# Kernel optimization log

Measured on AMD Instinct MI355X. Metric: run time of the kernel, lower is better.

## Reference

```python
import jax, jax.numpy as jnp
import numpy as np

N, E, K, NELEM, NB, NG = 10000, 160000, 64, 10, 8, 16
R_MAX = 5.0
P_CUT = 5
AVG_NEI = 16.0
SQRT4PI = 3.5449077018110318


def real_sph_l3(u):
    # real spherical harmonics up to l=3 (orthonormal), u: unit vectors [E,3]
    x, y, z = u[..., 0], u[..., 1], u[..., 2]
    x2, y2, z2 = x * x, y * y, z * z
    Y = [
        0.28209479177387814 * jnp.ones_like(x),
        0.4886025119029199 * y, 0.4886025119029199 * z, 0.4886025119029199 * x,
        1.0925484305920792 * x * y, 1.0925484305920792 * y * z,
        0.31539156525252005 * (3.0 * z2 - 1.0),
        1.0925484305920792 * x * z, 0.5462742152960396 * (x2 - y2),
        0.5900435899266435 * y * (3.0 * x2 - y2), 2.890611442640554 * x * y * z,
        0.4570457994644658 * y * (5.0 * z2 - 1.0), 0.3731763325901154 * z * (5.0 * z2 - 3.0),
        0.4570457994644658 * x * (5.0 * z2 - 1.0), 1.445305721320277 * z * (x2 - y2),
        0.5900435899266435 * x * (x2 - 3.0 * y2),
    ]
    return jnp.stack(Y, axis=-1)  # [E,16]


def radial_embed(r):
    # Bessel radial basis * polynomial cutoff (p=5)
    n = jnp.arange(1, NB + 1, dtype=r.dtype)
    pref = jnp.sqrt(2.0 / R_MAX)
    bessel = pref * jnp.sin(n[None, :] * jnp.pi * r[:, None] / R_MAX) / r[:, None]
    u = r / R_MAX
    fcut = 1.0 - 21.0 * u**5 + 35.0 * u**6 - 15.0 * u**7
    fcut = jnp.where(u < 1.0, fcut, 0.0)
    return bessel * fcut[:, None]  # [E,NB]


L_SLICES = [(0, 1), (1, 4), (4, 9), (9, 16)]


def product_basis(A, Wp):
    # many-body invariant (ACE-style) features per channel from A: [N,K,16]
    A0 = A[:, :, 0]                                         # nu=1 invariant
    p = jnp.stack([jnp.sum(A[:, :, a:b] ** 2, axis=-1) for a, b in L_SLICES], axis=-1)  # nu=2 power spectrum [N,K,4]
    cub = A0 * p.sum(axis=-1)                               # nu=3 invariant
    inv = jnp.concatenate([A0[..., None], p, cub[..., None]], axis=-1)  # [N,K,6]
    return jnp.einsum('nkj,kj->nk', inv, Wp)


def energy_fn(positions, node_attrs, shifts, atomic_energies, embed_W, Wr1, Wr2, lin_up, Wp, W_read, edge_index, batch):
    sender, receiver = edge_index[0], edge_index[1]
    vec = positions[receiver] - positions[sender] + shifts   # [E,3]
    r = jnp.sqrt(jnp.sum(vec * vec, axis=-1) + 1e-12)        # [E]
    sh = real_sph_l3(vec / r[:, None]) * SQRT4PI             # [E,16]
    rb = radial_embed(r)                                     # [E,NB]
    e0 = jax.ops.segment_sum(node_attrs @ atomic_energies, batch, num_segments=NG)
    h = node_attrs @ embed_W                                 # [N,K]
    for i in range(2):
        hu = h @ lin_up[i]                                   # [N,K]
        R = jax.nn.silu(rb @ Wr1[i]) @ Wr2[i]                # [E,K*16]
        R = R.reshape(E, K, 16)
        msg = R * sh[:, None, :] * hu[sender][:, :, None]    # [E,K,16]
        A = jax.ops.segment_sum(msg, receiver, num_segments=N) / AVG_NEI  # [N,K,16]
        h = product_basis(A, Wp[i])                          # [N,K]
    node_e = h @ W_read                                      # [N]
    inter_e = jax.ops.segment_sum(node_e, batch, num_segments=NG)
    return e0 + inter_e                                      # [NG]


def setup_inputs() -> dict:
    key = jax.random.key(0)
    ks = jax.random.split(key, 12)
    positions = jax.random.normal(ks[0], (N, 3), dtype=jnp.float32) * 2.0
    species = jax.random.randint(ks[1], (N,), 0, NELEM)
    node_attrs = jax.nn.one_hot(species, NELEM, dtype=jnp.float32)
    edge_index = jax.random.randint(ks[2], (2, E), 0, N)
    shifts = jnp.zeros((E, 3), dtype=jnp.float32)
    batch = jnp.sort(jax.random.randint(ks[3], (N,), 0, NG))
    atomic_energies = -jnp.arange(1.0, NELEM + 1.0, dtype=jnp.float32)
    s = 0.1
    embed_W = jax.random.normal(ks[4], (NELEM, K), dtype=jnp.float32) * s
    Wr1 = jax.random.normal(ks[5], (2, NB, 64), dtype=jnp.float32) * s
    Wr2 = jax.random.normal(ks[6], (2, 64, K * 16), dtype=jnp.float32) * s
    lin_up = jax.random.normal(ks[7], (2, K, K), dtype=jnp.float32) * s
    Wp = jax.random.normal(ks[8], (2, K, 6), dtype=jnp.float32) * s
    W_read = jax.random.normal(ks[9], (K,), dtype=jnp.float32) * s
    return {
        'positions': positions, 'node_attrs': node_attrs, 'shifts': shifts,
        'edge_index': edge_index, 'batch': batch, 'num_graphs': NG,
        'atomic_energies': atomic_energies, 'embed_W': embed_W, 'Wr1': Wr1,
        'Wr2': Wr2, 'lin_up': lin_up, 'Wp': Wp, 'W_read': W_read,
    }


def reference(positions, node_attrs, shifts, edge_index, batch, num_graphs,
              atomic_energies, embed_W, Wr1, Wr2, lin_up, Wp, W_read):
    def e_of_pos(pos):
        return energy_fn(pos, node_attrs, shifts, atomic_energies, embed_W,
                         Wr1, Wr2, lin_up, Wp, W_read, edge_index, batch)
    energy = e_of_pos(positions)
    forces = -jax.grad(lambda p: e_of_pos(p).sum())(positions)
    return energy, forces
```

## Files before the change

kernel.cpp:

```cpp
#include <hip/hip_runtime.h>
#include <cmath>
#include <type_traits>
#include <utility>

#define NA 10000
#define NE 160000
#define KC 64
#define NEL 10
#define NBR 8
#define NGR 16
#define ECH 16

#define C0 0.28209479177387814f
#define C1 0.4886025119029199f
#define C2 1.0925484305920792f
#define C3 0.31539156525252005f
#define C4 0.5462742152960396f
#define C5 0.5900435899266435f
#define C6 2.890611442640554f
#define C7 0.4570457994644658f
#define C8 0.3731763325901154f
#define C9 1.445305721320277f
#define SQ4PI 3.5449077018110318f
#define PREF 0.6324555320336759f
#define PI_F 3.14159265358979323846f

typedef float f32x4 __attribute__((ext_vector_type(4)));
typedef short s16x8 __attribute__((ext_vector_type(8)));
typedef __bf16 b16x8 __attribute__((ext_vector_type(8)));

__device__ __forceinline__ float sigmoidf_(float x){ return 1.0f/(1.0f+expf(-x)); }

__device__ __forceinline__ unsigned short f2b(float f){
  unsigned int u = __float_as_uint(f);
  unsigned int r = u + 0x7FFFu + ((u>>16)&1u);
  return (unsigned short)(r>>16);
}

template<typename T, typename = void>
struct mfma_takes_short : std::false_type {};
template<typename T>
struct mfma_takes_short<T, std::void_t<decltype(__builtin_amdgcn_mfma_f32_16x16x32_bf16(
    std::declval<T>(), std::declval<T>(), std::declval<f32x4>(), 0, 0, 0))>> : std::true_type {};

__device__ __forceinline__ f32x4 mfma16(s16x8 a, s16x8 b, f32x4 c){
  if constexpr (mfma_takes_short<s16x8>::value)
    return __builtin_amdgcn_mfma_f32_16x16x32_bf16(a, b, c, 0, 0, 0);
  else
    return __builtin_amdgcn_mfma_f32_16x16x32_bf16(
        __builtin_bit_cast(b16x8, a), __builtin_bit_cast(b16x8, b), c, 0, 0, 0);
}

__global__ void edge_geom_k(const float* __restrict__ pos, const float* __restrict__ shifts,
                            const int* __restrict__ eidx,
                            float* __restrict__ vecb, float* __restrict__ rbuf,
                            float* __restrict__ shb, float* __restrict__ rbb){
  int e = blockIdx.x*blockDim.x + threadIdx.x;
  if (e >= NE) return;
  int sn = eidx[e], rc = eidx[NE+e];
  float vx = pos[rc*3+0]-pos[sn*3+0]+shifts[e*3+0];
  float vy = pos[rc*3+1]-pos[sn*3+1]+shifts[e*3+1];
  float vz = pos[rc*3+2]-pos[sn*3+2]+shifts[e*3+2];
  float r = sqrtf(vx*vx+vy*vy+vz*vz+1e-12f);
  vecb[e*3+0]=vx; vecb[e*3+1]=vy; vecb[e*3+2]=vz; rbuf[e]=r;
  float inv = 1.0f/r; float x=vx*inv,y=vy*inv,z=vz*inv;
  float x2=x*x,y2=y*y,z2=z*z;
  float Y[16];
  Y[0]=C0; Y[1]=C1*y; Y[2]=C1*z; Y[3]=C1*x;
  Y[4]=C2*x*y; Y[5]=C2*y*z; Y[6]=C3*(3.f*z2-1.f); Y[7]=C2*x*z; Y[8]=C4*(x2-y2);
  Y[9]=C5*y*(3.f*x2-y2); Y[10]=C6*x*y*z; Y[11]=C7*y*(5.f*z2-1.f);
  Y[12]=C8*z*(5.f*z2-3.f); Y[13]=C7*x*(5.f*z2-1.f); Y[14]=C9*z*(x2-y2);
  Y[15]=C5*x*(x2-3.f*y2);
  #pragma unroll
  for (int m=0;m<16;m++) shb[e*16+m] = Y[m]*SQ4PI;
  float u = r*0.2f;
  float fc = 0.f;
  if (u < 1.0f){ float u2=u*u,u4=u2*u2,u5=u4*u,u6=u5*u,u7=u6*u; fc = 1.f-21.f*u5+35.f*u6-15.f*u7; }
  #pragma unroll
  for (int b=0;b<NBR;b++){
    float a = (float)(b+1)*PI_F*0.2f;
    rbb[e*NBR+b] = PREF*sinf(a*r)*inv*fc;
  }
}

__global__ void embed_k(const float* __restrict__ attrs, const float* __restrict__ W, float* __restrict__ h0){
  int idx = blockIdx.x*blockDim.x+threadIdx.x;
  if (idx >= NA*KC) return;
  int n = idx>>6, k = idx&63;
  float s=0;
  #pragma unroll
  for (int j=0;j<NEL;j++) s += attrs[n*NEL+j]*W[j*KC+k];
  h0[idx]=s;
}

__global__ void hu_k(const float* __restrict__ h, const float* __restrict__ lin, float* __restrict__ out){
  int idx = blockIdx.x*blockDim.x+threadIdx.x;
  if (idx >= NA*KC) return;
  int n = idx>>6, k = idx&63;
  float s=0;
  for (int c=0;c<KC;c++) s += h[n*KC+c]*lin[c*KC+k];
  out[idx]=s;
}

__global__ void ghu_to_gh_k(const float* __restrict__ g, const float* __restrict__ lin, float* __restrict__ out){
  int idx = blockIdx.x*blockDim.x+threadIdx.x;
  if (idx >= NA*KC) return;
  int n = idx>>6, k = idx&63;
  float s=0;
  for (int c=0;c<KC;c++) s += g[n*KC+c]*lin[k*KC+c];
  out[idx]=s;
}

__global__ void count_k(const int* __restrict__ eidx, int* __restrict__ cnt){
  int e = blockIdx.x*blockDim.x+threadIdx.x;
  if (e<NE) atomicAdd(&cnt[eidx[NE+e]], 1);
}
__global__ void scan_k(const int* __restrict__ cnt, int* __restrict__ rs, int* __restrict__ fill){
  __shared__ int part[256];
  int t = threadIdx.x;
  const int PER = (NA + 255)/256;
  int base = t*PER;
  int s = 0;
  for (int j=0;j<PER;j++){ int i=base+j; if (i<NA) s += cnt[i]; }
  part[t] = s; __syncthreads();
  for (int off=1; off<256; off<<=1){
    int v = (t>=off) ? part[t-off] : 0;
    __syncthreads();
    part[t] += v;
    __syncthreads();
  }
  int run = (t==0) ? 0 : part[t-1];
  for (int j=0;j<PER;j++){ int i=base+j; if (i<NA){ rs[i]=run; fill[i]=run; run += cnt[i]; } }
  if (t==255) rs[NA]=run;
}
__global__ void place_k(const int* __restrict__ eidx, int* __restrict__ fill, int* __restrict__ perm){
  int e = blockIdx.x*blockDim.x+threadIdx.x;
  if (e>=NE) return;
  int r = eidx[NE+e];
  int p = atomicAdd(&fill[r],1);
  perm[p]=e;
}

__global__ void prep_w_k(const float* __restrict__ Wr2, unsigned short* __restrict__ w2b,
                         unsigned short* __restrict__ w2t){
  int idx = blockIdx.x*blockDim.x+threadIdx.x;
  if (idx >= 2*65536) return;
  int l = idx>>16;
  int rem = idx & 65535;
  int c = rem>>10, o = rem&1023;
  unsigned short v = f2b(Wr2[idx]);
  w2b[idx] = v;
  w2t[l*65536 + o*64 + c] = v;
}

__global__ __launch_bounds__(256) void fwd_A_k(const int* __restrict__ rs, const int* __restrict__ perm,
    const int* __restrict__ eidx, const float* __restrict__ shb, const float* __restrict__ rbb,
    const float* __restrict__ hu, const float* __restrict__ Wr1, const unsigned short* __restrict__ w2t,
    float* __restrict__ A){
  __shared__ __align__(16) unsigned short s_s[16*64];
  __shared__ float s_sh[16*17];
  __shared__ float s_hu[16*68];
  __shared__ float s_rb[16*8];
  __shared__ float s_w1[8*64];
  __shared__ int s_snd[16];
  int n = blockIdx.x, t = threadIdx.x;
  int lane = t & 63, w = t >> 6;
  int row = lane & 15, g = lane >> 4;
  int e0 = rs[n], e1 = rs[n+1];
  s_w1[t] = Wr1[t]; s_w1[256+t] = Wr1[256+t];
  float acc[16];
  #pragma unroll
  for (int i=0;i<16;i++) acc[i]=0.f;

  for (int ce=e0; ce<e1; ce+=ECH){
    int ne = min(ECH, e1-ce);
    __syncthreads();
    if (t<ECH) s_snd[t] = (t<ne) ? eidx[perm[ce+t]] : -1;
    { int le=t>>4, m=t&15; s_sh[le*17+m] = (le<ne) ? shb[perm[ce+le]*16+m] : 0.f; }
    if (t < ECH*NBR){ int le=t>>3, b=t&7; s_rb[le*8+b] = (le<ne) ? rbb[perm[ce+le]*NBR+b] : 0.f; }
    __syncthreads();
    #pragma unroll
    for (int q=0;q<4;q++){
      int idx=q*256+t; int le=idx>>6, c=idx&63;
      int sn = s_snd[le];
      s_hu[le*68+c] = (sn>=0) ? hu[sn*KC+c] : 0.f;
      float tt=0;
      #pragma unroll
      for (int b=0;b<NBR;b++) tt += s_rb[le*8+b]*s_w1[b*64+c];
      float sv = tt*sigmoidf_(tt);
      s_s[le*64 + (c ^ ((le&7)<<3))] = (sn>=0) ? f2b(sv) : (unsigned short)0;
    }
    __syncthreads();
    s16x8 a0 = *(const s16x8*)&s_s[row*64 + ((g*8)      ^ ((row&7)<<3))];
    s16x8 a1 = *(const s16x8*)&s_s[row*64 + ((32 + g*8) ^ ((row&7)<<3))];
    #pragma unroll 4
    for (int ot=0; ot<16; ot++){
      int otile = w*16 + ot;
      const unsigned short* bp = w2t + (otile*16 + row)*64 + g*8;
      s16x8 b0 = *(const s16x8*)(bp);
      s16x8 b1 = *(const s16x8*)(bp + 32);
      f32x4 d = {0.f,0.f,0.f,0.f};
      d = mfma16(a0, b0, d);
      d = mfma16(a1, b1, d);
      float s = 0.f;
      #pragma unroll
      for (int q=0;q<4;q++){
        int e = g*4+q;
        s += d[q] * s_sh[e*17+row] * s_hu[e*68+otile];
      }
      acc[ot] += s;
    }
  }
  const float inv16 = 1.f/16.f;
  #pragma unroll
  for (int ot=0; ot<16; ot++){
    float v = acc[ot];
    v += __shfl_xor(v, 16);
    v += __shfl_xor(v, 32);
    if (lane < 16) A[n*1024 + (w*16+ot)*16 + lane] = v*inv16;
  }
}

__global__ void pb_fwd_k(const float* __restrict__ A, const float* __restrict__ Wp, float* __restrict__ h){
  int idx = blockIdx.x*blockDim.x+threadIdx.x;
  if (idx>=NA*KC) return;
  int k = idx&63;
  const float* a = A + idx*16;
  float v[16];
  #pragma unroll
  for (int m=0;m<16;m++) v[m]=a[m];
  float p0 = v[0]*v[0];
  float p1 = v[1]*v[1]+v[2]*v[2]+v[3]*v[3];
  float p2 = v[4]*v[4]+v[5]*v[5]+v[6]*v[6]+v[7]*v[7]+v[8]*v[8];
  float p3 = 0.f;
  #pragma unroll
  for (int m=9;m<16;m++) p3 += v[m]*v[m];
  float P = p0+p1+p2+p3;
  const float* wp = Wp + k*6;
  h[idx] = v[0]*wp[0] + p0*wp[1] + p1*wp[2] + p2*wp[3] + p3*wp[4] + v[0]*P*wp[5];
}

__global__ void pb_bwd_k(const float* __restrict__ A, const float* __restrict__ Wp,
                         const float* __restrict__ gh, const float* __restrict__ Wread,
                         int useW, float* __restrict__ gA){
  int idx = blockIdx.x*blockDim.x+threadIdx.x;
  if (idx>=NA*KC) return;
  int k = idx&63;
  const float* a = A + idx*16;
  float v[16];
  #pragma unroll
  for (int m=0;m<16;m++) v[m]=a[m];
  float p0 = v[0]*v[0];
  float p1 = v[1]*v[1]+v[2]*v[2]+v[3]*v[3];
  float p2 = v[4]*v[4]+v[5]*v[5]+v[6]*v[6]+v[7]*v[7]+v[8]*v[8];
  float p3 = 0.f;
  #pragma unroll
  for (int m=9;m<16;m++) p3 += v[m]*v[m];
  float P = p0+p1+p2+p3;
  float g = useW ? Wread[k] : gh[idx];
  const float* wp = Wp + k*6;
  float w5a0 = wp[5]*v[0];
  float out[16];
  #pragma unroll
  for (int m=0;m<16;m++){
    int l = (m==0)?0:(m<4)?1:(m<9)?2:3;
    float r = 2.f*v[m]*(wp[1+l] + w5a0);
    if (m==0) r += wp[0] + wp[5]*P;
    out[m] = g*r;
  }
  float* d = gA + idx*16;
  #pragma unroll
  for (int m=0;m<16;m++) d[m]=out[m];
}

__global__ __launch_bounds__(256) void bwd_edge_k(const int* __restrict__ eidx,
    const float* __restrict__ shb, const float* __restrict__ rbb,
    const float* __restrict__ vecb, const float* __restrict__ rbuf,
    const float* __restrict__ hu, const float* __restrict__ Wr1,
    const unsigned short* __restrict__ w2b,
    const unsigned short* __restrict__ w2t,
    const float* __restrict__ gA, float* __restrict__ ghu, int do_ghu,
    float* __restrict__ gpos){
  __shared__ __align__(16) unsigned short s_s[16*64];
  __shared__ __align__(16) unsigned short s_gR[16*1024];
  __shared__ float s_sh[16*17];
  __shared__ float s_hu[16*68];
  __shared__ float s_rb[16*8];
  __shared__ float s_w1[8*64];
  __shared__ float s_gshp[4*16*17];
  __shared__ float s_gt[16*64];
  __shared__ float s_grb[16*8];
  __shared__ int s_snd[16], s_rcv[16];
  int t = threadIdx.x, lane = t&63, w = t>>6;
  int row = lane&15, g = lane>>4;
  int eb = blockIdx.x*ECH;
  const float inv16 = 1.f/16.f;

  s_w1[t] = Wr1[t]; s_w1[256+t] = Wr1[256+t];
  if (t<ECH){ s_snd[t]=eidx[eb+t]; s_rcv[t]=eidx[NE+eb+t]; }
  { int le=t>>4, m=t&15; s_sh[le*17+m]=shb[(eb+le)*16+m]; }
  if (t<ECH*NBR){ int le=t>>3, b=t&7; s_rb[le*8+b]=rbb[(eb+le)*NBR+b]; }
  __syncthreads();
  #pragma unroll
  for (int q=0;q<4;q++){
    int idx=q*256+t; int le=idx>>6, c=idx&63;
    s_hu[le*68+c]=hu[s_snd[le]*KC+c];
    float tt=0;
    #pragma unroll
    for (int b=0;b<NBR;b++) tt += s_rb[le*8+b]*s_w1[b*64+c];
    s_s[le*64 + (c ^ ((le&7)<<3))] = f2b(tt*sigmoidf_(tt));
  }
  __syncthreads();

  s16x8 a0 = *(const s16x8*)&s_s[row*64 + ((g*8)      ^ ((row&7)<<3))];
  s16x8 a1 = *(const s16x8*)&s_s[row*64 + ((32 + g*8) ^ ((row&7)<<3))];
  float gsh_acc[4] = {0.f,0.f,0.f,0.f};
  #pragma unroll 2
  for (int ot=0; ot<16; ot++){
    int k = w*16 + ot;
    const unsigned short* bp = w2t + (k*16 + row)*64 + g*8;
    s16x8 b0 = *(const s16x8*)(bp);
    s16x8 b1 = *(const s16x8*)(bp + 32);
    f32x4 d = {0.f,0.f,0.f,0.f};
    d = mfma16(a0, b0, d);
    d = mfma16(a1, b1, d);
    float gm[4], ghv[4];
    #pragma unroll
    for (int q=0;q<4;q++) gm[q] = gA[s_rcv[g*4+q]*1024 + k*16 + row]*inv16;
    #pragma unroll
    for (int q=0;q<4;q++){
      int e = g*4+q;
      float shv = s_sh[e*17+row];
      float huv = s_hu[e*68+k];
      float p = gm[q]*d[q];
      ghv[q] = p*shv;
      gsh_acc[q] += p*huv;
      float gr = gm[q]*shv*huv;
      s_gR[e*1024 + ((k*16+row) ^ ((e&7)<<3))] = f2b(gr);
    }
    if (do_ghu){
      #pragma unroll
      for (int off=1; off<16; off<<=1){
        ghv[0]+=__shfl_xor(ghv[0],off); ghv[1]+=__shfl_xor(ghv[1],off);
        ghv[2]+=__shfl_xor(ghv[2],off); ghv[3]+=__shfl_xor(ghv[3],off);
      }
      if (row==0){
        #pragma unroll
        for (int q=0;q<4;q++) atomicAdd(&ghu[s_snd[g*4+q]*KC + k], ghv[q]);
      }
    }
  }
  #pragma unroll
  for (int q=0;q<4;q++) s_gshp[w*272 + (g*4+q)*17 + row] = gsh_acc[q];
  __syncthreads();

  f32x4 dgs = {0.f,0.f,0.f,0.f};
  #pragma unroll 4
  for (int kb=0; kb<32; kb++){
    int kelem = kb*32 + g*8;
    s16x8 a = *(const s16x8*)&s_gR[row*1024 + (kelem ^ ((row&7)<<3))];
    s16x8 b = *(const s16x8*)&w2b[(w*16+row)*1024 + kelem];
    dgs = mfma16(a, b, dgs);
  }
  #pragma unroll
  for (int q=0;q<4;q++){
    int e = g*4+q, c = w*16+row;
    float tt=0;
    #pragma unroll
    for (int b=0;b<NBR;b++) tt += s_rb[e*8+b]*s_w1[b*64+c];
    float sg = sigmoidf_(tt);
    float ds = sg*(1.f+tt*(1.f-sg));
    s_gt[e*64 + c] = dgs[q]*ds;
  }
  __syncthreads();

  if (t < ECH*NBR){
    int le=t>>3, b=t&7;
    float s=0;
    for (int c=0;c<KC;c++) s += s_gt[le*64+c]*s_w1[b*64+c];
    s_grb[le*8+b]=s;
  }
  { int le=t>>4, m=t&15;
    s_gshp[le*17+m] = s_gshp[le*17+m]+s_gshp[272+le*17+m]+s_gshp[544+le*17+m]+s_gshp[816+le*17+m]; }
  __syncthreads();

  if (t < ECH){
    int le=t; int e=eb+le;
    float r = rbuf[e]; float inv=1.f/r;
    float vx=vecb[e*3+0], vy=vecb[e*3+1], vz=vecb[e*3+2];
    float x=vx*inv, y=vy*inv, z=vz*inv;
    float x2=x*x, y2=y*y, z2=z*z;
    float G[16];
    #pragma unroll
    for (int m=0;m<16;m++) G[m]=s_gshp[le*17+m];
    float gx = C1*G[3] + C2*(y*G[4]+z*G[7]) + 2.f*C4*x*G[8] + 6.f*C5*x*y*G[9]
             + C6*y*z*G[10] + C7*(5.f*z2-1.f)*G[13] + 2.f*C9*x*z*G[14] + 3.f*C5*(x2-y2)*G[15];
    float gy = C1*G[1] + C2*(x*G[4]+z*G[5]) - 2.f*C4*y*G[8] + 3.f*C5*(x2-y2)*G[9]
             + C6*x*z*G[10] + C7*(5.f*z2-1.f)*G[11] - 2.f*C9*y*z*G[14] - 6.f*C5*x*y*G[15];
    float gz = C1*G[2] + C2*(y*G[5]+x*G[7]) + 6.f*C3*z*G[6] + C6*x*y*G[10]
             + 10.f*C7*y*z*G[11] + C8*(15.f*z2-3.f)*G[12] + 10.f*C7*x*z*G[13] + C9*(x2-y2)*G[14];
    gx*=SQ4PI; gy*=SQ4PI; gz*=SQ4PI;
    float gr=0.f;
    float u=r*0.2f;
    if (u<1.f){
      float u2=u*u, u4=u2*u2, u5=u4*u, u6=u5*u, u7=u6*u;
      float fc=1.f-21.f*u5+35.f*u6-15.f*u7;
      float dfc=(-105.f*u4+210.f*u5-105.f*u6)*0.2f;
      #pragma unroll
      for (int b=0;b<NBR;b++){
        float a=(float)(b+1)*PI_F*0.2f;
        float sa=sinf(a*r), ca=cosf(a*r);
        float bes=PREF*sa*inv;
        float dbes=PREF*(a*ca*inv - sa*inv*inv);
        gr += s_grb[le*8+b]*(dbes*fc + bes*dfc);
      }
    }
    float dot = x*gx+y*gy+z*gz;
    float gvx = (gx - x*dot)*inv + gr*x;
    float gvy = (gy - y*dot)*inv + gr*y;
    float gvz = (gz - z*dot)*inv + gr*z;
    int sn=s_snd[le], rc=s_rcv[le];
    atomicAdd(&gpos[rc*3+0], gvx); atomicAdd(&gpos[rc*3+1], gvy); atomicAdd(&gpos[rc*3+2], gvz);
    atomicAdd(&gpos[sn*3+0], -gvx); atomicAdd(&gpos[sn*3+1], -gvy); atomicAdd(&gpos[sn*3+2], -gvz);
  }
}

__global__ void energy_k(const float* __restrict__ attrs, const float* __restrict__ ae,
                         const float* __restrict__ h2, const float* __restrict__ Wread,
                         const int* __restrict__ batch, float* __restrict__ out_e){
  int n = blockIdx.x*blockDim.x+threadIdx.x;
  if (n>=NA) return;
  float v=0;
  #pragma unroll
  for (int j=0;j<NEL;j++) v += attrs[n*NEL+j]*ae[j];
  float s=0;
  for (int kk=0;kk<KC;kk++) s += h2[n*KC+kk]*Wread[kk];
  atomicAdd(&out_e[batch[n]], v+s);
}
__global__ void forces_k(const float* __restrict__ gpos, float* __restrict__ out_f){
  int i = blockIdx.x*blockDim.x+threadIdx.x;
  if (i<NA*3) out_f[i] = -gpos[i];
}

extern "C" void kernel_launch(void* const* d_in, const int* in_sizes, int n_in,
                              void* d_out, int out_size, void* d_ws, size_t ws_size,
                              hipStream_t stream){
  const float* pos    = (const float*)d_in[0];
  const float* attrs  = (const float*)d_in[1];
  const float* shifts = (const float*)d_in[2];
  const int*   eidx   = (const int*)d_in[3];
  const int*   batch  = (const int*)d_in[4];
  const float* ae     = (const float*)d_in[6];
  const float* embedW = (const float*)d_in[7];
  const float* Wr1    = (const float*)d_in[8];
  const float* Wr2    = (const float*)d_in[9];
  const float* lin    = (const float*)d_in[10];
  const float* Wp     = (const float*)d_in[11];
  const float* Wread  = (const float*)d_in[12];
  float* out_e = (float*)d_out;
  float* out_f = out_e + NGR;

  char* w = (char*)d_ws;
  auto alloc = [&](size_t nElem)->void*{ void* p = (void*)w; w += ((nElem*4 + 255)/256)*256; return p; };
  float* vecb = (float*)alloc((size_t)3*NE);
  float* rbuf = (float*)alloc((size_t)NE);
  float* shb  = (float*)alloc((size_t)16*NE);
  float* rbb  = (float*)alloc((size_t)8*NE);
  float* h0   = (float*)alloc((size_t)NA*KC);
  float* h1   = (float*)alloc((size_t)NA*KC);
  float* h2   = (float*)alloc((size_t)NA*KC);
  float* hu1  = (float*)alloc((size_t)NA*KC);
  float* hu2  = (float*)alloc((size_t)NA*KC);
  float* gh1  = (float*)alloc((size_t)NA*KC);
  float* ghu2 = (float*)alloc((size_t)NA*KC);
  float* A1   = (float*)alloc((size_t)NA*1024);
  float* A2   = (float*)alloc((size_t)NA*1024);
  float* gA   = (float*)alloc((size_t)NA*1024);
  float* gpos = (float*)alloc((size_t)NA*3);
  unsigned short* w2b = (unsigned short*)alloc((size_t)2*65536);
  unsigned short* w2t = (unsigned short*)alloc((size_t)2*65536);
  int* cnt  = (int*)alloc((size_t)NA);
  int* rsar = (int*)alloc((size_t)NA+1);
  int* fill = (int*)alloc((size_t)NA);
  int* perm = (int*)alloc((size_t)NE);

  hipMemsetAsync(cnt, 0, NA*sizeof(int), stream);
  hipMemsetAsync(gpos, 0, NA*3*sizeof(float), stream);
  hipMemsetAsync(ghu2, 0, NA*KC*sizeof(float), stream);
  hipMemsetAsync(out_e, 0, NGR*sizeof(float), stream);

  prep_w_k<<<(2*65536+255)/256, 256, 0, stream>>>(Wr2, w2b, w2t);
  edge_geom_k<<<(NE+255)/256, 256, 0, stream>>>(pos, shifts, eidx, vecb, rbuf, shb, rbb);
  embed_k<<<(NA*KC+255)/256, 256, 0, stream>>>(attrs, embedW, h0);
  count_k<<<(NE+255)/256, 256, 0, stream>>>(eidx, cnt);
  scan_k<<<1, 256, 0, stream>>>(cnt, rsar, fill);
  place_k<<<(NE+255)/256, 256, 0, stream>>>(eidx, fill, perm);

  hu_k<<<(NA*KC+255)/256, 256, 0, stream>>>(h0, lin + 0, hu1);
  fwd_A_k<<<NA, 256, 0, stream>>>(rsar, perm, eidx, shb, rbb, hu1, Wr1 + 0, w2t + 0, A1);
  pb_fwd_k<<<(NA*KC+255)/256, 256, 0, stream>>>(A1, Wp + 0, h1);
  hu_k<<<(NA*KC+255)/256, 256, 0, stream>>>(h1, lin + 4096, hu2);
  fwd_A_k<<<NA, 256, 0, stream>>>(rsar, perm, eidx, shb, rbb, hu2, Wr1 + 512, w2t + 65536, A2);
  pb_fwd_k<<<(NA*KC+255)/256, 256, 0, stream>>>(A2, Wp + 384, h2);

  energy_k<<<(NA+255)/256, 256, 0, stream>>>(attrs, ae, h2, Wread, batch, out_e);

  pb_bwd_k<<<(NA*KC+255)/256, 256, 0, stream>>>(A2, Wp + 384, (const float*)nullptr, Wread, 1, gA);
  bwd_edge_k<<<NE/ECH, 256, 0, stream>>>(eidx, shb, rbb, vecb, rbuf, hu2, Wr1 + 512, w2b + 65536, w2t + 65536, gA, ghu2, 1, gpos);
  ghu_to_gh_k<<<(NA*KC+255)/256, 256, 0, stream>>>(ghu2, lin + 4096, gh1);
  pb_bwd_k<<<(NA*KC+255)/256, 256, 0, stream>>>(A1, Wp + 0, gh1, (const float*)nullptr, 0, gA);
  bwd_edge_k<<<NE/ECH, 256, 0, stream>>>(eidx, shb, rbb, vecb, rbuf, hu1, Wr1 + 0, w2b + 0, w2t + 0, gA, (float*)nullptr, 0, gpos);

  forces_k<<<(NA*3+255)/256, 256, 0, stream>>>(gpos, out_f);
}
```

Before: 1.864 ms.

## Store edge data in receiver-sorted order and slice backward gradient staging

Edge geometry, spherical harmonics, radial basis and sender/receiver indices are now written directly at each edge's receiver-sorted position. The forward aggregation kernel can then read them contiguously instead of through a permutation. In the backward edge kernel, the 32KB shared gR buffer is split into four 8KB slices, each consumed by an MFMA pass right after it is produced. This cuts shared memory per block, which may raise occupancy, at the cost of extra barriers. Because backward edge blocks now group edges that share a receiver, the gA gathers hit the same rows, trading gather locality for more atomic contention on gpos.

Result: slower. 1.980 ms (+6.2%).

```diff
diff --git a/kernel.cpp b/kernel.cpp
--- a/kernel.cpp
+++ b/kernel.cpp
@@ -51,66 +51,6 @@
         __builtin_bit_cast(b16x8, a), __builtin_bit_cast(b16x8, b), c, 0, 0, 0);
 }
 
-__global__ void edge_geom_k(const float* __restrict__ pos, const float* __restrict__ shifts,
-                            const int* __restrict__ eidx,
-                            float* __restrict__ vecb, float* __restrict__ rbuf,
-                            float* __restrict__ shb, float* __restrict__ rbb){
-  int e = blockIdx.x*blockDim.x + threadIdx.x;
-  if (e >= NE) return;
-  int sn = eidx[e], rc = eidx[NE+e];
-  float vx = pos[rc*3+0]-pos[sn*3+0]+shifts[e*3+0];
-  float vy = pos[rc*3+1]-pos[sn*3+1]+shifts[e*3+1];
-  float vz = pos[rc*3+2]-pos[sn*3+2]+shifts[e*3+2];
-  float r = sqrtf(vx*vx+vy*vy+vz*vz+1e-12f);
-  vecb[e*3+0]=vx; vecb[e*3+1]=vy; vecb[e*3+2]=vz; rbuf[e]=r;
-  float inv = 1.0f/r; float x=vx*inv,y=vy*inv,z=vz*inv;
-  float x2=x*x,y2=y*y,z2=z*z;
-  float Y[16];
-  Y[0]=C0; Y[1]=C1*y; Y[2]=C1*z; Y[3]=C1*x;
-  Y[4]=C2*x*y; Y[5]=C2*y*z; Y[6]=C3*(3.f*z2-1.f); Y[7]=C2*x*z; Y[8]=C4*(x2-y2);
-  Y[9]=C5*y*(3.f*x2-y2); Y[10]=C6*x*y*z; Y[11]=C7*y*(5.f*z2-1.f);
-  Y[12]=C8*z*(5.f*z2-3.f); Y[13]=C7*x*(5.f*z2-1.f); Y[14]=C9*z*(x2-y2);
-  Y[15]=C5*x*(x2-3.f*y2);
-  #pragma unroll
-  for (int m=0;m<16;m++) shb[e*16+m] = Y[m]*SQ4PI;
-  float u = r*0.2f;
-  float fc = 0.f;
-  if (u < 1.0f){ float u2=u*u,u4=u2*u2,u5=u4*u,u6=u5*u,u7=u6*u; fc = 1.f-21.f*u5+35.f*u6-15.f*u7; }
-  #pragma unroll
-  for (int b=0;b<NBR;b++){
-    float a = (float)(b+1)*PI_F*0.2f;
-    rbb[e*NBR+b] = PREF*sinf(a*r)*inv*fc;
-  }
-}
-
-__global__ void embed_k(const float* __restrict__ attrs, const float* __restrict__ W, float* __restrict__ h0){
-  int idx = blockIdx.x*blockDim.x+threadIdx.x;
-  if (idx >= NA*KC) return;
-  int n = idx>>6, k = idx&63;
-  float s=0;
-  #pragma unroll
-  for (int j=0;j<NEL;j++) s += attrs[n*NEL+j]*W[j*KC+k];
-  h0[idx]=s;
-}
-
-__global__ void hu_k(const float* __restrict__ h, const float* __restrict__ lin, float* __restrict__ out){
-  int idx = blockIdx.x*blockDim.x+threadIdx.x;
-  if (idx >= NA*KC) return;
-  int n = idx>>6, k = idx&63;
-  float s=0;
-  for (int c=0;c<KC;c++) s += h[n*KC+c]*lin[c*KC+k];
-  out[idx]=s;
-}
-
-__global__ void ghu_to_gh_k(const float* __restrict__ g, const float* __restrict__ lin, float* __restrict__ out){
-  int idx = blockIdx.x*blockDim.x+threadIdx.x;
-  if (idx >= NA*KC) return;
-  int n = idx>>6, k = idx&63;
-  float s=0;
-  for (int c=0;c<KC;c++) s += g[n*KC+c]*lin[k*KC+c];
-  out[idx]=s;
-}
-
 __global__ void count_k(const int* __restrict__ eidx, int* __restrict__ cnt){
   int e = blockIdx.x*blockDim.x+threadIdx.x;
   if (e<NE) atomicAdd(&cnt[eidx[NE+e]], 1);
@@ -133,12 +73,75 @@
   for (int j=0;j<PER;j++){ int i=base+j; if (i<NA){ rs[i]=run; fill[i]=run; run += cnt[i]; } }
   if (t==255) rs[NA]=run;
 }
-__global__ void place_k(const int* __restrict__ eidx, int* __restrict__ fill, int* __restrict__ perm){
+__global__ void place_k(const int* __restrict__ eidx, int* __restrict__ fill, int* __restrict__ prank){
   int e = blockIdx.x*blockDim.x+threadIdx.x;
   if (e>=NE) return;
   int r = eidx[NE+e];
   int p = atomicAdd(&fill[r],1);
-  perm[p]=e;
+  prank[e]=p;
+}
+
+__global__ void edge_geom_k(const float* __restrict__ pos, const float* __restrict__ shifts,
+                            const int* __restrict__ eidx, const int* __restrict__ prank,
+                            float* __restrict__ vecb, float* __restrict__ rbuf,
+                            float* __restrict__ shb, float* __restrict__ rbb,
+                            int* __restrict__ sndp, int* __restrict__ rcvp){
+  int e = blockIdx.x*blockDim.x + threadIdx.x;
+  if (e >= NE) return;
+  int sn = eidx[e], rc = eidx[NE+e];
+  int p = prank[e];
+  float vx = pos[rc*3+0]-pos[sn*3+0]+shifts[e*3+0];
+  float vy = pos[rc*3+1]-pos[sn*3+1]+shifts[e*3+1];
+  float vz = pos[rc*3+2]-pos[sn*3+2]+shifts[e*3+2];
+  float r = sqrtf(vx*vx+vy*vy+vz*vz+1e-12f);
+  vecb[p*3+0]=vx; vecb[p*3+1]=vy; vecb[p*3+2]=vz; rbuf[p]=r;
+  sndp[p]=sn; rcvp[p]=rc;
+  float inv = 1.0f/r; float x=vx*inv,y=vy*inv,z=vz*inv;
+  float x2=x*x,y2=y*y,z2=z*z;
+  float Y[16];
+  Y[0]=C0; Y[1]=C1*y; Y[2]=C1*z; Y[3]=C1*x;
+  Y[4]=C2*x*y; Y[5]=C2*y*z; Y[6]=C3*(3.f*z2-1.f); Y[7]=C2*x*z; Y[8]=C4*(x2-y2);
+  Y[9]=C5*y*(3.f*x2-y2); Y[10]=C6*x*y*z; Y[11]=C7*y*(5.f*z2-1.f);
+  Y[12]=C8*z*(5.f*z2-3.f); Y[13]=C7*x*(5.f*z2-1.f); Y[14]=C9*z*(x2-y2);
+  Y[15]=C5*x*(x2-3.f*y2);
+  #pragma unroll
+  for (int m=0;m<16;m++) shb[p*16+m] = Y[m]*SQ4PI;
+  float u = r*0.2f;
+  float fc = 0.f;
+  if (u < 1.0f){ float u2=u*u,u4=u2*u2,u5=u4*u,u6=u5*u,u7=u6*u; fc = 1.f-21.f*u5+35.f*u6-15.f*u7; }
+  #pragma unroll
+  for (int b=0;b<NBR;b++){
+    float a = (float)(b+1)*PI_F*0.2f;
+    rbb[p*NBR+b] = PREF*sinf(a*r)*inv*fc;
+  }
+}
+
+__global__ void embed_k(const float* __restrict__ attrs, const float* __restrict__ W, float* __restrict__ h0){
+  int idx = blockIdx.x*blockDim.x+threadIdx.x;
+  if (idx >= NA*KC) return;
+  int n = idx>>6, k = idx&63;
+  float s=0;
+  #pragma unroll
+  for (int j=0;j<NEL;j++) s += attrs[n*NEL+j]*W[j*KC+k];
+  h0[idx]=s;
+}
+
+__global__ void hu_k(const float* __restrict__ h, const float* __restrict__ lin, float* __restrict__ out){
+  int idx = blockIdx.x*blockDim.x+threadIdx.x;
+  if (idx >= NA*KC) return;
+  int n = idx>>6, k = idx&63;
+  float s=0;
+  for (int c=0;c<KC;c++) s += h[n*KC+c]*lin[c*KC+k];
+  out[idx]=s;
+}
+
+__global__ void ghu_to_gh_k(const float* __restrict__ g, const float* __restrict__ lin, float* __restrict__ out){
+  int idx = blockIdx.x*blockDim.x+threadIdx.x;
+  if (idx >= NA*KC) return;
+  int n = idx>>6, k = idx&63;
+  float s=0;
+  for (int c=0;c<KC;c++) s += g[n*KC+c]*lin[k*KC+c];
+  out[idx]=s;
 }
 
 __global__ void prep_w_k(const float* __restrict__ Wr2, unsigned short* __restrict__ w2b,
@@ -153,8 +156,8 @@
   w2t[l*65536 + o*64 + c] = v;
 }
 
-__global__ __launch_bounds__(256) void fwd_A_k(const int* __restrict__ rs, const int* __restrict__ perm,
-    const int* __restrict__ eidx, const float* __restrict__ shb, const float* __restrict__ rbb,
+__global__ __launch_bounds__(256) void fwd_A_k(const int* __restrict__ rs,
+    const int* __restrict__ sndp, const float* __restrict__ shb, const float* __restrict__ rbb,
     const float* __restrict__ hu, const float* __restrict__ Wr1, const unsigned short* __restrict__ w2t,
     float* __restrict__ A){
   __shared__ __align__(16) unsigned short s_s[16*64];
@@ -175,9 +178,9 @@
   for (int ce=e0; ce<e1; ce+=ECH){
     int ne = min(ECH, e1-ce);
     __syncthreads();
-    if (t<ECH) s_snd[t] = (t<ne) ? eidx[perm[ce+t]] : -1;
-    { int le=t>>4, m=t&15; s_sh[le*17+m] = (le<ne) ? shb[perm[ce+le]*16+m] : 0.f; }
-    if (t < ECH*NBR){ int le=t>>3, b=t&7; s_rb[le*8+b] = (le<ne) ? rbb[perm[ce+le]*NBR+b] : 0.f; }
+    if (t<ECH) s_snd[t] = (t<ne) ? sndp[ce+t] : -1;
+    { int le=t>>4, m=t&15; s_sh[le*17+m] = (le<ne) ? shb[(ce+le)*16+m] : 0.f; }
+    if (t < ECH*NBR){ int le=t>>3, b=t&7; s_rb[le*8+b] = (le<ne) ? rbb[(ce+le)*NBR+b] : 0.f; }
     __syncthreads();
     #pragma unroll
     for (int q=0;q<4;q++){
@@ -273,7 +276,8 @@
   for (int m=0;m<16;m++) d[m]=out[m];
 }
 
-__global__ __launch_bounds__(256) void bwd_edge_k(const int* __restrict__ eidx,
+__global__ __launch_bounds__(256) void bwd_edge_k(
+    const int* __restrict__ sndp, const int* __restrict__ rcvp,
     const float* __restrict__ shb, const float* __restrict__ rbb,
     const float* __restrict__ vecb, const float* __restrict__ rbuf,
     const float* __restrict__ hu, const float* __restrict__ Wr1,
@@ -282,7 +286,7 @@
     const float* __restrict__ gA, float* __restrict__ ghu, int do_ghu,
     float* __restrict__ gpos){
   __shared__ __align__(16) unsigned short s_s[16*64];
-  __shared__ __align__(16) unsigned short s_gR[16*1024];
+  __shared__ __align__(16) unsigned short s_gRs[16*256];
   __shared__ float s_sh[16*17];
   __shared__ float s_hu[16*68];
   __shared__ float s_rb[16*8];
@@ -297,7 +301,7 @@
   const float inv16 = 1.f/16.f;
 
   s_w1[t] = Wr1[t]; s_w1[256+t] = Wr1[256+t];
-  if (t<ECH){ s_snd[t]=eidx[eb+t]; s_rcv[t]=eidx[NE+eb+t]; }
+  if (t<ECH){ s_snd[t]=sndp[eb+t]; s_rcv[t]=rcvp[eb+t]; }
   { int le=t>>4, m=t&15; s_sh[le*17+m]=shb[(eb+le)*16+m]; }
   if (t<ECH*NBR){ int le=t>>3, b=t&7; s_rb[le*8+b]=rbb[(eb+le)*NBR+b]; }
   __syncthreads();
@@ -315,53 +319,56 @@
   s16x8 a0 = *(const s16x8*)&s_s[row*64 + ((g*8)      ^ ((row&7)<<3))];
   s16x8 a1 = *(const s16x8*)&s_s[row*64 + ((32 + g*8) ^ ((row&7)<<3))];
   float gsh_acc[4] = {0.f,0.f,0.f,0.f};
-  #pragma unroll 2
-  for (int ot=0; ot<16; ot++){
-    int k = w*16 + ot;
-    const unsigned short* bp = w2t + (k*16 + row)*64 + g*8;
-    s16x8 b0 = *(const s16x8*)(bp);
-    s16x8 b1 = *(const s16x8*)(bp + 32);
-    f32x4 d = {0.f,0.f,0.f,0.f};
-    d = mfma16(a0, b0, d);
-    d = mfma16(a1, b1, d);
-    float gm[4], ghv[4];
+  f32x4 dgs = {0.f,0.f,0.f,0.f};
+
+  for (int sl=0; sl<4; sl++){
     #pragma unroll
-    for (int q=0;q<4;q++) gm[q] = gA[s_rcv[g*4+q]*1024 + k*16 + row]*inv16;
-    #pragma unroll
-    for (int q=0;q<4;q++){
-      int e = g*4+q;
-      float shv = s_sh[e*17+row];
-      float huv = s_hu[e*68+k];
-      float p = gm[q]*d[q];
-      ghv[q] = p*shv;
-      gsh_acc[q] += p*huv;
-      float gr = gm[q]*shv*huv;
-      s_gR[e*1024 + ((k*16+row) ^ ((e&7)<<3))] = f2b(gr);
-    }
-    if (do_ghu){
+    for (int j=0;j<4;j++){
+      int k = sl*16 + w*4 + j;
+      const unsigned short* bp = w2t + (k*16 + row)*64 + g*8;
+      s16x8 b0 = *(const s16x8*)(bp);
+      s16x8 b1 = *(const s16x8*)(bp + 32);
+      f32x4 d = {0.f,0.f,0.f,0.f};
+      d = mfma16(a0, b0, d);
+      d = mfma16(a1, b1, d);
+      int lo = (w*4+j)*16 + row;
+      float gm[4], ghv[4];
       #pragma unroll
-      for (int off=1; off<16; off<<=1){
-        ghv[0]+=__shfl_xor(ghv[0],off); ghv[1]+=__shfl_xor(ghv[1],off);
-        ghv[2]+=__shfl_xor(ghv[2],off); ghv[3]+=__shfl_xor(ghv[3],off);
+      for (int q=0;q<4;q++) gm[q] = gA[(size_t)s_rcv[g*4+q]*1024 + k*16 + row]*inv16;
+      #pragma unroll
+      for (int q=0;q<4;q++){
+        int e = g*4+q;
+        float shv = s_sh[e*17+row];
+        float huv = s_hu[e*68+k];
+        float p = gm[q]*d[q];
+        ghv[q] = p*shv;
+        gsh_acc[q] += p*huv;
+        float gr = gm[q]*shv*huv;
+        s_gRs[e*256 + (lo ^ ((e&7)<<3))] = f2b(gr);
       }
-      if (row==0){
+      if (do_ghu){
         #pragma unroll
-        for (int q=0;q<4;q++) atomicAdd(&ghu[s_snd[g*4+q]*KC + k], ghv[q]);
+        for (int off=1; off<16; off<<=1){
+          ghv[0]+=__shfl_xor(ghv[0],off); ghv[1]+=__shfl_xor(ghv[1],off);
+          ghv[2]+=__shfl_xor(ghv[2],off); ghv[3]+=__shfl_xor(ghv[3],off);
+        }
+        if (row==0){
+          #pragma unroll
+          for (int q=0;q<4;q++) atomicAdd(&ghu[s_snd[g*4+q]*KC + k], ghv[q]);
+        }
       }
     }
-  }
-  #pragma unroll
-  for (int q=0;q<4;q++) s_gshp[w*272 + (g*4+q)*17 + row] = gsh_acc[q];
-  __syncthreads();
-
-  f32x4 dgs = {0.f,0.f,0.f,0.f};
-  #pragma unroll 4
-  for (int kb=0; kb<32; kb++){
-    int kelem = kb*32 + g*8;
-    s16x8 a = *(const s16x8*)&s_gR[row*1024 + (kelem ^ ((row&7)<<3))];
-    s16x8 b = *(const s16x8*)&w2b[(w*16+row)*1024 + kelem];
-    dgs = mfma16(a, b, dgs);
-  }
+    __syncthreads();
+    #pragma unroll
+    for (int kb=0; kb<8; kb++){
+      int lk = kb*32 + g*8;
+      s16x8 a = *(const s16x8*)&s_gRs[row*256 + (lk ^ ((row&7)<<3))];
+      s16x8 b = *(const s16x8*)&w2b[(w*16+row)*1024 + sl*256 + lk];
+      dgs = mfma16(a, b, dgs);
+    }
+    __syncthreads();
+  }
+
   #pragma unroll
   for (int q=0;q<4;q++){
     int e = g*4+q, c = w*16+row;
@@ -372,6 +379,8 @@
     float ds = sg*(1.f+tt*(1.f-sg));
     s_gt[e*64 + c] = dgs[q]*ds;
   }
+  #pragma unroll
+  for (int q=0;q<4;q++) s_gshp[w*272 + (g*4+q)*17 + row] = gsh_acc[q];
   __syncthreads();
 
   if (t < ECH*NBR){
@@ -385,9 +394,9 @@
   __syncthreads();
 
   if (t < ECH){
-    int le=t; int e=eb+le;
-    float r = rbuf[e]; float inv=1.f/r;
-    float vx=vecb[e*3+0], vy=vecb[e*3+1], vz=vecb[e*3+2];
+    int le=t; int p=eb+le;
+    float r = rbuf[p]; float inv=1.f/r;
+    float vx=vecb[p*3+0], vy=vecb[p*3+1], vz=vecb[p*3+2];
     float x=vx*inv, y=vy*inv, z=vz*inv;
     float x2=x*x, y2=y*y, z2=z*z;
     float G[16];
@@ -482,34 +491,37 @@
   int* cnt  = (int*)alloc((size_t)NA);
   int* rsar = (int*)alloc((size_t)NA+1);
   int* fill = (int*)alloc((size_t)NA);
-  int* perm = (int*)alloc((size_t)NE);
+  int* prank= (int*)alloc((size_t)NE);
+  int* sndp = (int*)alloc((size_t)NE);
+  int* rcvp = (int*)alloc((size_t)NE);
 
   hipMemsetAsync(cnt, 0, NA*sizeof(int), stream);
   hipMemsetAsync(gpos, 0, NA*3*sizeof(float), stream);
   hipMemsetAsync(ghu2, 0, NA*KC*sizeof(float), stream);
   hipMemsetAsync(out_e, 0, NGR*sizeof(float), stream);
 
-  prep_w_k<<<(2*65536+255)/256, 256, 0, stream>>>(Wr2, w2b, w2t);
-  edge_geom_k<<<(NE+255)/256, 256, 0, stream>>>(pos, shifts, eidx, vecb, rbuf, shb, rbb);
-  embed_k<<<(NA*KC+255)/256, 256, 0, stream>>>(attrs, embedW, h0);
   count_k<<<(NE+255)/256, 256, 0, stream>>>(eidx, cnt);
   scan_k<<<1, 256, 0, stream>>>(cnt, rsar, fill);
-  place_k<<<(NE+255)/256, 256, 0, stream>>>(eidx, fill, perm);
+  place_k<<<(NE+255)/256, 256, 0, stream>>>(eidx, fill, prank);
+
+  prep_w_k<<<(2*65536+255)/256, 256, 0, stream>>>(Wr2, w2b, w2t);
+  edge_geom_k<<<(NE+255)/256, 256, 0, stream>>>(pos, shifts, eidx, prank, vecb, rbuf, shb, rbb, sndp, rcvp);
+  embed_k<<<(NA*KC+255)/256, 256, 0, stream>>>(attrs, embedW, h0);
 
   hu_k<<<(NA*KC+255)/256, 256, 0, stream>>>(h0, lin + 0, hu1);
-  fwd_A_k<<<NA, 256, 0, stream>>>(rsar, perm, eidx, shb, rbb, hu1, Wr1 + 0, w2t + 0, A1);
+  fwd_A_k<<<NA, 256, 0, stream>>>(rsar, sndp, shb, rbb, hu1, Wr1 + 0, w2t + 0, A1);
   pb_fwd_k<<<(NA*KC+255)/256, 256, 0, stream>>>(A1, Wp + 0, h1);
   hu_k<<<(NA*KC+255)/256, 256, 0, stream>>>(h1, lin + 4096, hu2);
-  fwd_A_k<<<NA, 256, 0, stream>>>(rsar, perm, eidx, shb, rbb, hu2, Wr1 + 512, w2t + 65536, A2);
+  fwd_A_k<<<NA, 256, 0, stream>>>(rsar, sndp, shb, rbb, hu2, Wr1 + 512, w2t + 65536, A2);
   pb_fwd_k<<<(NA*KC+255)/256, 256, 0, stream>>>(A2, Wp + 384, h2);
 
   energy_k<<<(NA+255)/256, 256, 0, stream>>>(attrs, ae, h2, Wread, batch, out_e);
 
   pb_bwd_k<<<(NA*KC+255)/256, 256, 0, stream>>>(A2, Wp + 384, (const float*)nullptr, Wread, 1, gA);
-  bwd_edge_k<<<NE/ECH, 256, 0, stream>>>(eidx, shb, rbb, vecb, rbuf, hu2, Wr1 + 512, w2b + 65536, w2t + 65536, gA, ghu2, 1, gpos);
+  bwd_edge_k<<<NE/ECH, 256, 0, stream>>>(sndp, rcvp, shb, rbb, vecb, rbuf, hu2, Wr1 + 512, w2b + 65536, w2t + 65536, gA, ghu2, 1, gpos);
   ghu_to_gh_k<<<(NA*KC+255)/256, 256, 0, stream>>>(ghu2, lin + 4096, gh1);
   pb_bwd_k<<<(NA*KC+255)/256, 256, 0, stream>>>(A1, Wp + 0, gh1, (const float*)nullptr, 0, gA);
-  bwd_edge_k<<<NE/ECH, 256, 0, stream>>>(eidx, shb, rbb, vecb, rbuf, hu1, Wr1 + 0, w2b + 0, w2t + 0, gA, (float*)nullptr, 0, gpos);
+  bwd_edge_k<<<NE/ECH, 256, 0, stream>>>(sndp, rcvp, shb, rbb, vecb, rbuf, hu1, Wr1 + 0, w2b + 0, w2t + 0, gA, (float*)nullptr, 0, gpos);
 
   forces_k<<<(NA*3+255)/256, 256, 0, stream>>>(gpos, out_f);
 }
```
